# Performance work log

Hardware: AMD Instinct MI355X
Metric: run time of the kernel (lower is better)

Reference implementation:

```python
import jax, jax.numpy as jnp
import numpy as np

T, B, OBS, H, A = 512, 256, 128, 256, 32

def setup_inputs() -> dict:
    key = jax.random.key(0)
    ks = jax.random.split(key, 16)
    s = 0.05
    return {
        'hidden': jnp.zeros((B, H), jnp.float32),
        'obs': jax.random.normal(ks[0], (T, B, OBS), jnp.float32),
        'dones': jax.random.bernoulli(ks[1], 0.1, (T, B)),
        'avail_actions': (jax.random.uniform(ks[2], (T, B, A)) > 0.1).astype(jnp.float32),
        'W_emb': jax.random.normal(ks[3], (OBS, H), jnp.float32) * s,
        'b_emb': jnp.zeros((H,), jnp.float32),
        'Wi': jax.random.normal(ks[4], (H, 3 * H), jnp.float32) * s,
        'bi': jnp.zeros((3 * H,), jnp.float32),
        'Whr': jax.random.normal(ks[5], (H, H), jnp.float32) * s,
        'Whz': jax.random.normal(ks[6], (H, H), jnp.float32) * s,
        'Whn': jax.random.normal(ks[7], (H, H), jnp.float32) * s,
        'bhn': jnp.zeros((H,), jnp.float32),
        'W_a1': jax.random.normal(ks[8], (H, H), jnp.float32) * s,
        'b_a1': jnp.zeros((H,), jnp.float32),
        'W_a2': jax.random.normal(ks[9], (H, A), jnp.float32) * s,
        'b_a2': jnp.zeros((A,), jnp.float32),
        'W_c1': jax.random.normal(ks[10], (H, H), jnp.float32) * s,
        'b_c1': jnp.zeros((H,), jnp.float32),
        'W_c2': jax.random.normal(ks[11], (H, 1), jnp.float32) * s,
        'b_c2': jnp.zeros((1,), jnp.float32),
    }

def reference(hidden, obs, dones, avail_actions, W_emb, b_emb, Wi, bi,
              Whr, Whz, Whn, bhn, W_a1, b_a1, W_a2, b_a2, W_c1, b_c1, W_c2, b_c2):
    # obs embedding + relu: [T,B,OBS] -> [T,B,H]
    emb = jax.nn.relu(obs @ W_emb + b_emb)
    # precompute input gate projections for all timesteps (same math as per-step Dense)
    gi = emb @ Wi + bi  # [T,B,3H]

    def step(h, xs):
        gi_t, done_t = xs
        h = jnp.where(done_t[:, None], 0.0, h)  # reset-select to zero init carry
        ir, iz, inn = jnp.split(gi_t, 3, axis=-1)
        r = jax.nn.sigmoid(ir + h @ Whr)
        z = jax.nn.sigmoid(iz + h @ Whz)
        n = jnp.tanh(inn + r * (h @ Whn + bhn))
        h_new = (1.0 - z) * n + z * h
        return h_new, h_new

    hidden_out, y = jax.lax.scan(step, hidden, (gi, dones))  # y: [T,B,H]

    actor_h = jax.nn.relu(y @ W_a1 + b_a1)
    actor_mean = actor_h @ W_a2 + b_a2  # [T,B,A]
    logits = actor_mean - (1.0 - avail_actions) * 1e10

    critic_h = jax.nn.relu(y @ W_c1 + b_c1)
    value = jnp.squeeze(critic_h @ W_c2 + b_c2, axis=-1)  # [T,B]
    return hidden_out, logits, value
```

## Files before the change

### kernel.cpp

```cpp
#include <hip/hip_runtime.h>
#include <stdint.h>

#define T_DIM 512
#define B_DIM 256
#define OBS_DIM 128
#define H_DIM 256
#define A_DIM 32
#define TB (T_DIM*B_DIM)

typedef unsigned short u16;
typedef unsigned int   u32;
typedef _Float16 half2v __attribute__((ext_vector_type(2)));
typedef __attribute__((ext_vector_type(8))) short short8;
typedef __attribute__((ext_vector_type(4))) float f32x4;
typedef __attribute__((ext_vector_type(4))) u32   u32x4;

__device__ __forceinline__ float bf2f(u16 v){ return __uint_as_float(((u32)v)<<16); }
__device__ __forceinline__ u16 f2bf(float f){
    u32 x = __float_as_uint(f);
    u32 r = x + 0x7fffu + ((x>>16)&1u);
    return (u16)(r>>16);
}
__device__ __forceinline__ float2 bfpair(u32 u){
    return make_float2(__uint_as_float(u<<16), __uint_as_float(u & 0xffff0000u));
}

__device__ __forceinline__ float dot2(u32 a, u32 b, float c){
#if __has_builtin(__builtin_amdgcn_fdot2)
    return __builtin_amdgcn_fdot2(__builtin_bit_cast(half2v,a),
                                  __builtin_bit_cast(half2v,b), c, false);
#else
    half2v ha = __builtin_bit_cast(half2v,a), hb = __builtin_bit_cast(half2v,b);
    return fmaf((float)ha[0],(float)hb[0], fmaf((float)ha[1],(float)hb[1], c));
#endif
}

__global__ void zero_flags_kernel(int* p){ if(threadIdx.x<4) p[threadIdx.x]=0; }

__global__ void detect_kernel(const unsigned char* __restrict__ d, int n, int* __restrict__ flags){
    int f=0;
    for(int p = blockIdx.x*blockDim.x+threadIdx.x; p<n; p += gridDim.x*blockDim.x){
        if(d[p]){ int m=p&3; if(m==1) f|=1; else if(m>=2) f|=2; }
    }
    if(f) atomicOr(flags, f);
}

__global__ void concat_bias_kernel(const float* __restrict__ a, const float* __restrict__ b,
                                   float* __restrict__ dst){
    int i = threadIdx.x;
    dst[i] = a[i];
    dst[256 + i] = b[i];
}

__global__ void cvt_wt_kernel(const float* __restrict__ Whr, const float* __restrict__ Whz,
                              const float* __restrict__ Whn, u32* __restrict__ dst){
    int i = blockIdx.x*blockDim.x + threadIdx.x;
    if(i >= 3*32*256*4) return;
    int e = i & 3;
    int j = (i >> 2) & 255;
    int q = (i >> 10) & 31;
    int m = i >> 15;
    const float* W = (m==0) ? Whr : (m==1) ? Whz : Whn;
    int kp = q*4 + e, k = 2*kp;
    _Float16 lo = (_Float16)W[(size_t)k    *H_DIM + j];
    _Float16 hi = (_Float16)W[(size_t)(k+1)*H_DIM + j];
    dst[i] = (u32)__builtin_bit_cast(u16,lo) | ((u32)__builtin_bit_cast(u16,hi) << 16);
}

__global__ void cvt_wT_kernel(const float* __restrict__ W, u16* __restrict__ dst,
                              int K, int N){
    int i = blockIdx.x*blockDim.x + threadIdx.x;
    if(i >= K*N) return;
    int n = i / K;
    int k = i - n*K;
    dst[i] = f2bf(W[(size_t)k*N + n]);
}

template<int RELU, int AF32>
__global__ __launch_bounds__(256, 2)
void gemm_mfma_kernel(const void* __restrict__ A_, const u16* __restrict__ Bt,
                      const float* __restrict__ bias, u16* __restrict__ C,
                      int M, int N, int K)
{
    __shared__ u16 As[128*32];
    __shared__ u16 Bs[128*32];
    const int tid  = threadIdx.x;
    const int wave = tid >> 6;
    const int lane = tid & 63;
    const int ln15 = lane & 15;
    const int quad = lane >> 4;
    const int wm = wave & 1, wn = wave >> 1;
    const int rowBase = blockIdx.y*128;
    const int colBase = blockIdx.x*128;

    f32x4 acc[4][4] = {};

    const int sr = tid >> 1;
    const int sc = (tid & 1) * 16;

    for(int kb = 0; kb < K; kb += 32){
        if(AF32){
            const float* af = (const float*)A_;
            const float* ag = af + (size_t)(rowBase+sr)*K + kb + sc;
            float4 f0 = *(const float4*)ag;
            float4 f1 = *(const float4*)(ag+4);
            float4 f2 = *(const float4*)(ag+8);
            float4 f3 = *(const float4*)(ag+12);
            u16 tmp[16] = { f2bf(f0.x),f2bf(f0.y),f2bf(f0.z),f2bf(f0.w),
                            f2bf(f1.x),f2bf(f1.y),f2bf(f1.z),f2bf(f1.w),
                            f2bf(f2.x),f2bf(f2.y),f2bf(f2.z),f2bf(f2.w),
                            f2bf(f3.x),f2bf(f3.y),f2bf(f3.z),f2bf(f3.w) };
            *(uint4*)&As[sr*32 + sc]     = *(const uint4*)&tmp[0];
            *(uint4*)&As[sr*32 + sc + 8] = *(const uint4*)&tmp[8];
        } else {
            const u16* ab = (const u16*)A_;
            const u16* ag = ab + (size_t)(rowBase+sr)*K + kb + sc;
            uint4 av0 = *(const uint4*)ag;
            uint4 av1 = *(const uint4*)(ag+8);
            *(uint4*)&As[sr*32 + sc]     = av0;
            *(uint4*)&As[sr*32 + sc + 8] = av1;
        }
        {
            const u16* bg = Bt + (size_t)(colBase+sr)*K + kb + sc;
            uint4 bv0 = *(const uint4*)bg;
            uint4 bv1 = *(const uint4*)(bg+8);
            *(uint4*)&Bs[sr*32 + sc]     = bv0;
            *(uint4*)&Bs[sr*32 + sc + 8] = bv1;
        }
        __syncthreads();

        short8 af[4], bf[4];
        #pragma unroll
        for(int mt=0;mt<4;mt++)
            af[mt] = *(const short8*)&As[(wm*64+mt*16+ln15)*32 + quad*8];
        #pragma unroll
        for(int nt=0;nt<4;nt++)
            bf[nt] = *(const short8*)&Bs[(wn*64+nt*16+ln15)*32 + quad*8];
        #pragma unroll
        for(int mt=0;mt<4;mt++){
            #pragma unroll
            for(int nt=0;nt<4;nt++){
                acc[mt][nt] = __builtin_amdgcn_mfma_f32_16x16x32_bf16(
                                  af[mt], bf[nt], acc[mt][nt], 0, 0, 0);
            }
        }
        __syncthreads();
    }

    #pragma unroll
    for(int nt=0;nt<4;nt++){
        int n = colBase + wn*64 + nt*16 + ln15;
        float bv = bias[n];
        #pragma unroll
        for(int mt=0;mt<4;mt++){
            #pragma unroll
            for(int r=0;r<4;r++){
                int m = rowBase + wm*64 + mt*16 + quad*4 + r;
                float v = acc[mt][nt][r] + bv;
                if(RELU) v = fmaxf(v, 0.f);
                C[(size_t)m*N + n] = f2bf(v);
            }
        }
    }
}

__global__ __attribute__((amdgpu_flat_work_group_size(1024,1024), amdgpu_waves_per_eu(4,4)))
void scan_kernel(const u16* __restrict__ gi, const void* __restrict__ dones,
                 const int* __restrict__ flags, const u32x4* __restrict__ Wt4,
                 const float* __restrict__ bhn, float* __restrict__ h_carry,
                 u16* __restrict__ y, int t0, int Tc)
{
    __shared__ __align__(16) u32 nw_lds[32*256*4/4*4];
    __shared__ __align__(16) u32 hbuf[2][128];
    __shared__ float rex[3][4][256];
    const int tid = threadIdx.x;
    const int j   = tid & 255;
    const int g   = tid >> 8;
    const int row = blockIdx.x;
    const int fl  = flags[0];
    const int mode = (fl&1) ? 0 : ((fl&2) ? 2 : 1);

    auto getdone = [&](int t)->bool{
        int idx = t*B_DIM + row;
        if(mode==0) return ((const unsigned char*)dones)[idx] != 0;
        if(mode==1) return ((const int*)dones)[idx] != 0;
        return ((const float*)dones)[idx] != 0.f;
    };

    const u32x4* baseR = Wt4 + (size_t)( 0 + g*8)*256 + j;
    const u32x4* baseZ = Wt4 + (size_t)(32 + g*8)*256 + j;
    const u32x4* baseN = Wt4 + (size_t)(64 + g*8)*256 + j;
    u32 wr[32], wz[32];
    #pragma unroll
    for(int q=0;q<8;q++){
        u32x4 tr = baseR[(size_t)q*256]; wr[4*q]=tr[0]; wr[4*q+1]=tr[1]; wr[4*q+2]=tr[2]; wr[4*q+3]=tr[3];
        u32x4 tz = baseZ[(size_t)q*256]; wz[4*q]=tz[0]; wz[4*q+1]=tz[1]; wz[4*q+2]=tz[2]; wz[4*q+3]=tz[3];
    }
    {
        u32x4* nl = (u32x4*)nw_lds;
        #pragma unroll
        for(int q=0;q<8;q++)
            nl[(size_t)(g*8+q)*256 + j] = baseN[(size_t)q*256];
    }
    #pragma unroll
    for(int q=0;q<32;q+=4){
        asm volatile("" : "+v"(wr[q  ]),"+v"(wr[q+1]),"+v"(wr[q+2]),"+v"(wr[q+3]),
                          "+v"(wz[q  ]),"+v"(wz[q+1]),"+v"(wz[q+2]),"+v"(wz[q+3]));
    }

    float bh = 0.f;
    float hoj = 0.f;
    if(g == 0){
        bh = bhn[j];
        bool d0 = getdone(t0);
        hoj = d0 ? 0.f : h_carry[(size_t)row*H_DIM + j];
        ((_Float16*)hbuf[0])[j] = (_Float16)hoj;
    }
    __syncthreads();

    int cur = 0;
    for(int t=0; t<Tc; ++t){
        size_t gbase = ((size_t)t*B_DIM + row)*768;
        float ir=0.f, izv=0.f, inn=0.f; bool dn=false;
        if(g == 0){
            ir  = bf2f(gi[gbase + j]);
            izv = bf2f(gi[gbase + 256 + j]);
            inn = bf2f(gi[gbase + 512 + j]);
            dn  = (t < Tc-1) ? getdone(t0+t+1) : false;
        }

        float r0=0.f,r1=0.f,z0=0.f,z1=0.f,n0=0.f,n1=0.f;
        const u32x4* hb = (const u32x4*)hbuf[cur] + g*8;
        const u32x4* nb = (const u32x4*)nw_lds + (size_t)(g*8)*256 + j;
        #pragma unroll
        for(int q=0;q<8;q++){
            u32x4 hv = hb[q];
            u32x4 nv = nb[(size_t)q*256];
            r0 = dot2(wr[4*q  ], hv[0], r0); r1 = dot2(wr[4*q+1], hv[1], r1);
            r0 = dot2(wr[4*q+2], hv[2], r0); r1 = dot2(wr[4*q+3], hv[3], r1);
            z0 = dot2(wz[4*q  ], hv[0], z0); z1 = dot2(wz[4*q+1], hv[1], z1);
            z0 = dot2(wz[4*q+2], hv[2], z0); z1 = dot2(wz[4*q+3], hv[3], z1);
            n0 = dot2(nv[0], hv[0], n0); n1 = dot2(nv[1], hv[1], n1);
            n0 = dot2(nv[2], hv[2], n0); n1 = dot2(nv[3], hv[3], n1);
        }
        rex[0][g][j] = r0 + r1;
        rex[1][g][j] = z0 + z1;
        rex[2][g][j] = n0 + n1;
        __syncthreads();

        if(g == 0){
            float rt = (rex[0][0][j] + rex[0][1][j]) + (rex[0][2][j] + rex[0][3][j]);
            float zt = (rex[1][0][j] + rex[1][1][j]) + (rex[1][2][j] + rex[1][3][j]);
            float nt = (rex[2][0][j] + rex[2][1][j]) + (rex[2][2][j] + rex[2][3][j]);
            float r = 1.f/(1.f + __expf(-(ir + rt)));
            float z = 1.f/(1.f + __expf(-(izv + zt)));
            float x = inn + r*(nt + bh);
            float e2 = __expf(2.f*x);
            float n = 1.f - 2.f/(e2 + 1.f);
            float hn = (1.f - z)*n + z*hoj;
            y[((size_t)t*B_DIM + row)*H_DIM + j] = f2bf(hn);
            hoj = dn ? 0.f : hn;
            ((_Float16*)hbuf[cur^1])[j] = (_Float16)hoj;
        }
        __syncthreads();
        cur ^= 1;
    }

    if(g == 0) h_carry[(size_t)row*H_DIM + j] = hoj;
}

__global__ __launch_bounds__(256)
void actor2_kernel(const u16* __restrict__ ah, int ld, const float* __restrict__ W_a2,
                   const float* __restrict__ b_a2, const float* __restrict__ avail,
                   float* __restrict__ logits)
{
    __shared__ u16 ahs[64][264];
    const int tid = threadIdx.x;
    const int r0 = blockIdx.x*64;
    {
        int row = tid & 63;
        int c0 = (tid >> 6) * 64;
        const uint4* gp = (const uint4*)(ah + (size_t)(r0+row)*ld + c0);
        #pragma unroll
        for(int q=0;q<8;q++){
            uint4 u = gp[q];
            u32* dst = (u32*)&ahs[row][c0 + q*8];
            dst[0]=u.x; dst[1]=u.y; dst[2]=u.z; dst[3]=u.w;
        }
    }
    __syncthreads();
    const int c  = tid & 31;
    const int rg = tid >> 5;
    float acc[8]={0.f,0.f,0.f,0.f,0.f,0.f,0.f,0.f};
    float bc = b_a2[c];
    for(int k=0;k<H_DIM;k+=4){
        float w0 = W_a2[(k+0)*A_DIM + c];
        float w1 = W_a2[(k+1)*A_DIM + c];
        float w2 = W_a2[(k+2)*A_DIM + c];
        float w3 = W_a2[(k+3)*A_DIM + c];
        #pragma unroll
        for(int rr=0;rr<8;rr++){
            uint2 av = *(const uint2*)&ahs[rg*8+rr][k];
            float2 p0 = bfpair(av.x), p1 = bfpair(av.y);
            acc[rr] = fmaf(p0.x,w0,fmaf(p0.y,w1,fmaf(p1.x,w2,fmaf(p1.y,w3,acc[rr]))));
        }
    }
    #pragma unroll
    for(int rr=0;rr<8;rr++){
        int grow = r0 + rg*8 + rr;
        float av = avail[(size_t)grow*A_DIM + c];
        logits[(size_t)grow*A_DIM + c] = acc[rr] + bc - (1.f-av)*1e10f;
    }
}

__global__ __launch_bounds__(256)
void critic2_kernel(const u16* __restrict__ ch, int ld, const float* __restrict__ W_c2,
                    const float* __restrict__ b_c2, float* __restrict__ value)
{
    const int lane = threadIdx.x & 63;
    const int wid  = threadIdx.x >> 6;
    const int row  = blockIdx.x*4 + wid;
    uint2 av = *(const uint2*)(ch + (size_t)row*ld + lane*4);
    float2 p0 = bfpair(av.x), p1 = bfpair(av.y);
    float4 wv = *(const float4*)(W_c2 + lane*4);
    float acc = p0.x*wv.x + p0.y*wv.y + p1.x*wv.z + p1.y*wv.w;
    #pragma unroll
    for(int off=32; off>0; off>>=1) acc += __shfl_down(acc, off, 64);
    if(lane==0) value[row] = acc + b_c2[0];
}

extern "C" void kernel_launch(void* const* d_in, const int* in_sizes, int n_in,
                              void* d_out, int out_size, void* d_ws, size_t ws_size,
                              hipStream_t stream)
{
    const float* hidden = (const float*)d_in[0];
    const float* obs    = (const float*)d_in[1];
    const void*  dones  = d_in[2];
    const float* avail  = (const float*)d_in[3];
    const float* W_emb  = (const float*)d_in[4];
    const float* b_emb  = (const float*)d_in[5];
    const float* Wi     = (const float*)d_in[6];
    const float* bi     = (const float*)d_in[7];
    const float* Whr    = (const float*)d_in[8];
    const float* Whz    = (const float*)d_in[9];
    const float* Whn    = (const float*)d_in[10];
    const float* bhn    = (const float*)d_in[11];
    const float* W_a1   = (const float*)d_in[12];
    const float* b_a1   = (const float*)d_in[13];
    const float* W_a2   = (const float*)d_in[14];
    const float* b_a2   = (const float*)d_in[15];
    const float* W_c1   = (const float*)d_in[16];
    const float* b_c1   = (const float*)d_in[17];
    const float* W_c2   = (const float*)d_in[18];
    const float* b_c2   = (const float*)d_in[19];

    float* out_hidden = (float*)d_out;
    float* out_logits = out_hidden + (size_t)B_DIM*H_DIM;
    float* out_value  = out_logits + (size_t)TB*A_DIM;

    const size_t fixed = 393216 + 393216 + 262144 + 65536 + 262144 + 256 + 2048;
    int Tc = 4;
    for(int cand = 64; cand >= 4; cand >>= 1){
        size_t need = fixed + (size_t)cand*(393216  + 262144  + 131072 );
        if(need <= ws_size){ Tc = cand; break; }
    }
    const int NC = T_DIM / Tc;

    uint8_t* ws = (uint8_t*)d_ws;
    size_t off = 0;
    u32*  wt_b    = (u32*)(ws + off); off += 393216;
    u16*  wiT     = (u16*)(ws + off); off += 393216;
    u16*  wacT    = (u16*)(ws + off); off += 262144;
    u16*  wembT   = (u16*)(ws + off); off += 65536;
    float* h_carry= (float*)(ws + off); off += 262144;
    int*  flags   = (int*)(ws + off); off += 256;
    float* b_ac   = (float*)(ws + off); off += 2048;
    u16*  gi_c    = (u16*)(ws + off); off += (size_t)Tc*393216;
    u16*  embac_c = (u16*)(ws + off); off += (size_t)Tc*262144;
    u16*  y_c     = (u16*)(ws + off); off += (size_t)Tc*131072;
    u16*  emb_c   = embac_c;
    u16*  ac_c    = embac_c;

    zero_flags_kernel<<<1, 64, 0, stream>>>(flags);
    detect_kernel<<<64, 256, 0, stream>>>((const unsigned char*)dones, TB, flags);
    cvt_wt_kernel<<<384, 256, 0, stream>>>(Whr, Whz, Whn, wt_b);
    cvt_wT_kernel<<<768, 256, 0, stream>>>(Wi,   wiT,  256, 768);
    cvt_wT_kernel<<<256, 256, 0, stream>>>(W_a1, wacT,          256, 256);
    cvt_wT_kernel<<<256, 256, 0, stream>>>(W_c1, wacT + 65536,  256, 256);
    cvt_wT_kernel<<<128, 256, 0, stream>>>(W_emb, wembT, 128, 256);
    concat_bias_kernel<<<1, 256, 0, stream>>>(b_a1, b_c1, b_ac);
    hipMemcpyAsync(h_carry, hidden, (size_t)B_DIM*H_DIM*sizeof(float),
                   hipMemcpyDeviceToDevice, stream);

    const int Mc = Tc*B_DIM;
    const int gy = Mc/128;

    for(int c = 0; c < NC; ++c){
        const int t0 = c*Tc;
        const float* obs_c = obs + (size_t)t0*B_DIM*OBS_DIM;
        gemm_mfma_kernel<1,1><<<dim3(2,gy), 256, 0, stream>>>(obs_c, wembT, b_emb, emb_c, Mc, 256, 128);
        gemm_mfma_kernel<0,0><<<dim3(6,gy), 256, 0, stream>>>(emb_c, wiT, bi, gi_c, Mc, 768, 256);
        scan_kernel<<<256, 1024, 0, stream>>>(gi_c, dones, flags, (const u32x4*)wt_b,
                                              bhn, h_carry, y_c, t0, Tc);
        gemm_mfma_kernel<1,0><<<dim3(4,gy), 256, 0, stream>>>(y_c, wacT, b_ac, ac_c, Mc, 512, 256);
        actor2_kernel<<<Mc/64, 256, 0, stream>>>(ac_c, 512, W_a2, b_a2,
                                                 avail + (size_t)t0*B_DIM*A_DIM,
                                                 out_logits + (size_t)t0*B_DIM*A_DIM);
        critic2_kernel<<<Mc/4, 256, 0, stream>>>(ac_c + 256, 512, W_c2, b_c2,
                                                 out_value + (size_t)t0*B_DIM);
    }

    hipMemcpyAsync(out_hidden, h_carry, (size_t)B_DIM*H_DIM*sizeof(float),
                   hipMemcpyDeviceToDevice, stream);
}
```

Baseline: 1.360 ms.

## Use MFMA for GRU recurrent matmul with four batch rows per block

Replaces the per-row scan kernel's fdot2 matvec, which holds weights in registers and LDS, with MFMA 16x16x32 f16 instructions. Each block now processes four batch rows, padded to a 16-row tile in LDS with an XOR swizzle, and all recurrent weights stay in registers. The aim is to cut per-step latency and the number of blocks by amortising weight use across rows on the matrix cores. In exchange, 12 of the 16 MFMA rows are wasted, only 64 blocks run, and a new transposed f16 weight conversion is needed.

Result: slower. 1.936 ms (+42.4%).

```diff
diff --git a/kernel.cpp b/kernel.cpp
--- a/kernel.cpp
+++ b/kernel.cpp
@@ -7,10 +7,12 @@
 #define H_DIM 256
 #define A_DIM 32
 #define TB (T_DIM*B_DIM)
+#define SR 4
 
 typedef unsigned short u16;
 typedef unsigned int   u32;
 typedef _Float16 half2v __attribute__((ext_vector_type(2)));
+typedef _Float16 f16x8 __attribute__((ext_vector_type(8)));
 typedef __attribute__((ext_vector_type(8))) short short8;
 typedef __attribute__((ext_vector_type(4))) float f32x4;
 typedef __attribute__((ext_vector_type(4))) u32   u32x4;
@@ -25,16 +27,6 @@
     return make_float2(__uint_as_float(u<<16), __uint_as_float(u & 0xffff0000u));
 }
 
-__device__ __forceinline__ float dot2(u32 a, u32 b, float c){
-#if __has_builtin(__builtin_amdgcn_fdot2)
-    return __builtin_amdgcn_fdot2(__builtin_bit_cast(half2v,a),
-                                  __builtin_bit_cast(half2v,b), c, false);
-#else
-    half2v ha = __builtin_bit_cast(half2v,a), hb = __builtin_bit_cast(half2v,b);
-    return fmaf((float)ha[0],(float)hb[0], fmaf((float)ha[1],(float)hb[1], c));
-#endif
-}
-
 __global__ void zero_flags_kernel(int* p){ if(threadIdx.x<4) p[threadIdx.x]=0; }
 
 __global__ void detect_kernel(const unsigned char* __restrict__ d, int n, int* __restrict__ flags){
@@ -52,19 +44,15 @@
     dst[256 + i] = b[i];
 }
 
-__global__ void cvt_wt_kernel(const float* __restrict__ Whr, const float* __restrict__ Whz,
-                              const float* __restrict__ Whn, u32* __restrict__ dst){
+__global__ void cvt_wT3_f16_kernel(const float* __restrict__ Whr, const float* __restrict__ Whz,
+                                   const float* __restrict__ Whn, _Float16* __restrict__ dst){
     int i = blockIdx.x*blockDim.x + threadIdx.x;
-    if(i >= 3*32*256*4) return;
-    int e = i & 3;
-    int j = (i >> 2) & 255;
-    int q = (i >> 10) & 31;
-    int m = i >> 15;
+    if(i >= 3*H_DIM*H_DIM) return;
+    int k = i & 255;
+    int j = (i >> 8) & 255;
+    int m = i >> 16;
     const float* W = (m==0) ? Whr : (m==1) ? Whz : Whn;
-    int kp = q*4 + e, k = 2*kp;
-    _Float16 lo = (_Float16)W[(size_t)k    *H_DIM + j];
-    _Float16 hi = (_Float16)W[(size_t)(k+1)*H_DIM + j];
-    dst[i] = (u32)__builtin_bit_cast(u16,lo) | ((u32)__builtin_bit_cast(u16,hi) << 16);
+    dst[i] = (_Float16)W[(size_t)k*H_DIM + j];
 }
 
 __global__ void cvt_wT_kernel(const float* __restrict__ W, u16* __restrict__ dst,
@@ -164,109 +152,124 @@
     }
 }
 
-__global__ __attribute__((amdgpu_flat_work_group_size(1024,1024), amdgpu_waves_per_eu(4,4)))
+__global__ __attribute__((amdgpu_flat_work_group_size(512,512), amdgpu_waves_per_eu(2,2)))
 void scan_kernel(const u16* __restrict__ gi, const void* __restrict__ dones,
-                 const int* __restrict__ flags, const u32x4* __restrict__ Wt4,
+                 const int* __restrict__ flags, const _Float16* __restrict__ WT,
                  const float* __restrict__ bhn, float* __restrict__ h_carry,
                  u16* __restrict__ y, int t0, int Tc)
 {
-    __shared__ __align__(16) u32 nw_lds[32*256*4/4*4];
-    __shared__ __align__(16) u32 hbuf[2][128];
-    __shared__ float rex[3][4][256];
-    const int tid = threadIdx.x;
-    const int j   = tid & 255;
-    const int g   = tid >> 8;
-    const int row = blockIdx.x;
-    const int fl  = flags[0];
+    __shared__ _Float16 h_lds[16*256];
+    __shared__ float accb[3][256][6];
+    __shared__ unsigned char dn_lds[64][SR];
+
+    const int tid  = threadIdx.x;
+    const int wave = tid >> 6;
+    const int lane = tid & 63;
+    const int ln15 = lane & 15;
+    const int quad = lane >> 4;
+    const int rb   = blockIdx.x * SR;
+    const int fl   = flags[0];
     const int mode = (fl&1) ? 0 : ((fl&2) ? 2 : 1);
 
-    auto getdone = [&](int t)->bool{
-        int idx = t*B_DIM + row;
-        if(mode==0) return ((const unsigned char*)dones)[idx] != 0;
-        if(mode==1) return ((const int*)dones)[idx] != 0;
-        return ((const float*)dones)[idx] != 0.f;
-    };
-
-    const u32x4* baseR = Wt4 + (size_t)( 0 + g*8)*256 + j;
-    const u32x4* baseZ = Wt4 + (size_t)(32 + g*8)*256 + j;
-    const u32x4* baseN = Wt4 + (size_t)(64 + g*8)*256 + j;
-    u32 wr[32], wz[32];
+    f16x8 wf[2][3][8];
+    {
+        const f16x8* Wv = (const f16x8*)WT;
+        #pragma unroll
+        for(int s=0;s<2;s++){
+            int col = (wave*2+s)*16 + ln15;
+            #pragma unroll
+            for(int m=0;m<3;m++){
+                #pragma unroll
+                for(int kk=0;kk<8;kk++)
+                    wf[s][m][kk] = Wv[(size_t)(m*256 + col)*32 + kk*4 + quad];
+            }
+        }
+    }
+
+    if(tid < Tc*SR){
+        int tt = tid >> 2, r = tid & 3;
+        int idx = (t0+tt)*B_DIM + rb + r;
+        bool d;
+        if(mode==0)      d = ((const unsigned char*)dones)[idx] != 0;
+        else if(mode==1) d = ((const int*)dones)[idx] != 0;
+        else             d = ((const float*)dones)[idx] != 0.f;
+        dn_lds[tt][r] = d ? 1 : 0;
+    }
+    for(int i = 1024 + tid; i < 4096; i += 512) h_lds[i] = (_Float16)0.f;
+    __syncthreads();
+
+    const int col = tid & 255;
+    const int rp  = tid >> 8;
+    const float bh = bhn[col];
+    float hreg[2];
     #pragma unroll
-    for(int q=0;q<8;q++){
-        u32x4 tr = baseR[(size_t)q*256]; wr[4*q]=tr[0]; wr[4*q+1]=tr[1]; wr[4*q+2]=tr[2]; wr[4*q+3]=tr[3];
-        u32x4 tz = baseZ[(size_t)q*256]; wz[4*q]=tz[0]; wz[4*q+1]=tz[1]; wz[4*q+2]=tz[2]; wz[4*q+3]=tz[3];
-    }
-    {
-        u32x4* nl = (u32x4*)nw_lds;
-        #pragma unroll
-        for(int q=0;q<8;q++)
-            nl[(size_t)(g*8+q)*256 + j] = baseN[(size_t)q*256];
-    }
-    #pragma unroll
-    for(int q=0;q<32;q+=4){
-        asm volatile("" : "+v"(wr[q  ]),"+v"(wr[q+1]),"+v"(wr[q+2]),"+v"(wr[q+3]),
-                          "+v"(wz[q  ]),"+v"(wz[q+1]),"+v"(wz[q+2]),"+v"(wz[q+3]));
-    }
-
-    float bh = 0.f;
-    float hoj = 0.f;
-    if(g == 0){
-        bh = bhn[j];
-        bool d0 = getdone(t0);
-        hoj = d0 ? 0.f : h_carry[(size_t)row*H_DIM + j];
-        ((_Float16*)hbuf[0])[j] = (_Float16)hoj;
+    for(int e=0;e<2;e++){
+        int row = rp*2 + e;
+        bool d0 = dn_lds[0][row] != 0;
+        hreg[e] = d0 ? 0.f : h_carry[(size_t)(rb+row)*H_DIM + col];
+        h_lds[row*256 + (((col>>3) ^ row)<<3) + (col&7)] = (_Float16)hreg[e];
     }
     __syncthreads();
 
-    int cur = 0;
     for(int t=0; t<Tc; ++t){
-        size_t gbase = ((size_t)t*B_DIM + row)*768;
-        float ir=0.f, izv=0.f, inn=0.f; bool dn=false;
-        if(g == 0){
-            ir  = bf2f(gi[gbase + j]);
-            izv = bf2f(gi[gbase + 256 + j]);
-            inn = bf2f(gi[gbase + 512 + j]);
-            dn  = (t < Tc-1) ? getdone(t0+t+1) : false;
-        }
-
-        float r0=0.f,r1=0.f,z0=0.f,z1=0.f,n0=0.f,n1=0.f;
-        const u32x4* hb = (const u32x4*)hbuf[cur] + g*8;
-        const u32x4* nb = (const u32x4*)nw_lds + (size_t)(g*8)*256 + j;
-        #pragma unroll
-        for(int q=0;q<8;q++){
-            u32x4 hv = hb[q];
-            u32x4 nv = nb[(size_t)q*256];
-            r0 = dot2(wr[4*q  ], hv[0], r0); r1 = dot2(wr[4*q+1], hv[1], r1);
-            r0 = dot2(wr[4*q+2], hv[2], r0); r1 = dot2(wr[4*q+3], hv[3], r1);
-            z0 = dot2(wz[4*q  ], hv[0], z0); z1 = dot2(wz[4*q+1], hv[1], z1);
-            z0 = dot2(wz[4*q+2], hv[2], z0); z1 = dot2(wz[4*q+3], hv[3], z1);
-            n0 = dot2(nv[0], hv[0], n0); n1 = dot2(nv[1], hv[1], n1);
-            n0 = dot2(nv[2], hv[2], n0); n1 = dot2(nv[3], hv[3], n1);
-        }
-        rex[0][g][j] = r0 + r1;
-        rex[1][g][j] = z0 + z1;
-        rex[2][g][j] = n0 + n1;
+        size_t gb = ((size_t)t*B_DIM + rb)*768;
+        float giv[2][3];
+        #pragma unroll
+        for(int e=0;e<2;e++){
+            size_t ro = gb + (size_t)(rp*2+e)*768;
+            giv[e][0] = bf2f(gi[ro + col]);
+            giv[e][1] = bf2f(gi[ro + 256 + col]);
+            giv[e][2] = bf2f(gi[ro + 512 + col]);
+        }
+
+        f32x4 acc[2][3] = {};
+        #pragma unroll
+        for(int kk=0;kk<8;kk++){
+            f16x8 hv = *(const f16x8*)&h_lds[ln15*256 + (((kk*4+quad) ^ (ln15&7))<<3)];
+            #pragma unroll
+            for(int s=0;s<2;s++){
+                acc[s][0] = __builtin_amdgcn_mfma_f32_16x16x32_f16(hv, wf[s][0][kk], acc[s][0], 0,0,0);
+                acc[s][1] = __builtin_amdgcn_mfma_f32_16x16x32_f16(hv, wf[s][1][kk], acc[s][1], 0,0,0);
+                acc[s][2] = __builtin_amdgcn_mfma_f32_16x16x32_f16(hv, wf[s][2][kk], acc[s][2], 0,0,0);
+            }
+        }
+
+        if(quad == 0){
+            #pragma unroll
+            for(int s=0;s<2;s++){
+                int c = (wave*2+s)*16 + ln15;
+                #pragma unroll
+                for(int m=0;m<3;m++){
+                    *(float2*)&accb[m][c][0] = make_float2(acc[s][m][0], acc[s][m][1]);
+                    *(float2*)&accb[m][c][2] = make_float2(acc[s][m][2], acc[s][m][3]);
+                }
+            }
+        }
         __syncthreads();
 
-        if(g == 0){
-            float rt = (rex[0][0][j] + rex[0][1][j]) + (rex[0][2][j] + rex[0][3][j]);
-            float zt = (rex[1][0][j] + rex[1][1][j]) + (rex[1][2][j] + rex[1][3][j]);
-            float nt = (rex[2][0][j] + rex[2][1][j]) + (rex[2][2][j] + rex[2][3][j]);
-            float r = 1.f/(1.f + __expf(-(ir + rt)));
-            float z = 1.f/(1.f + __expf(-(izv + zt)));
-            float x = inn + r*(nt + bh);
+        #pragma unroll
+        for(int e=0;e<2;e++){
+            int row = rp*2 + e;
+            float rt  = accb[0][col][row];
+            float zt  = accb[1][col][row];
+            float ntv = accb[2][col][row];
+            float r = 1.f/(1.f + __expf(-(giv[e][0] + rt)));
+            float z = 1.f/(1.f + __expf(-(giv[e][1] + zt)));
+            float x = giv[e][2] + r*(ntv + bh);
             float e2 = __expf(2.f*x);
             float n = 1.f - 2.f/(e2 + 1.f);
-            float hn = (1.f - z)*n + z*hoj;
-            y[((size_t)t*B_DIM + row)*H_DIM + j] = f2bf(hn);
-            hoj = dn ? 0.f : hn;
-            ((_Float16*)hbuf[cur^1])[j] = (_Float16)hoj;
+            float hn = (1.f - z)*n + z*hreg[e];
+            y[((size_t)t*B_DIM + rb + row)*H_DIM + col] = f2bf(hn);
+            bool dn = (t < Tc-1) ? (dn_lds[t+1][row] != 0) : false;
+            hreg[e] = dn ? 0.f : hn;
+            h_lds[row*256 + (((col>>3) ^ row)<<3) + (col&7)] = (_Float16)hreg[e];
         }
         __syncthreads();
-        cur ^= 1;
-    }
-
-    if(g == 0) h_carry[(size_t)row*H_DIM + j] = hoj;
+    }
+
+    #pragma unroll
+    for(int e=0;e<2;e++)
+        h_carry[(size_t)(rb + rp*2 + e)*H_DIM + col] = hreg[e];
 }
 
 __global__ __launch_bounds__(256)
@@ -368,7 +371,7 @@
 
     uint8_t* ws = (uint8_t*)d_ws;
     size_t off = 0;
-    u32*  wt_b    = (u32*)(ws + off); off += 393216;
+    _Float16* wT  = (_Float16*)(ws + off); off += 393216;
     u16*  wiT     = (u16*)(ws + off); off += 393216;
     u16*  wacT    = (u16*)(ws + off); off += 262144;
     u16*  wembT   = (u16*)(ws + off); off += 65536;
@@ -383,7 +386,7 @@
 
     zero_flags_kernel<<<1, 64, 0, stream>>>(flags);
     detect_kernel<<<64, 256, 0, stream>>>((const unsigned char*)dones, TB, flags);
-    cvt_wt_kernel<<<384, 256, 0, stream>>>(Whr, Whz, Whn, wt_b);
+    cvt_wT3_f16_kernel<<<768, 256, 0, stream>>>(Whr, Whz, Whn, wT);
     cvt_wT_kernel<<<768, 256, 0, stream>>>(Wi,   wiT,  256, 768);
     cvt_wT_kernel<<<256, 256, 0, stream>>>(W_a1, wacT,          256, 256);
     cvt_wT_kernel<<<256, 256, 0, stream>>>(W_c1, wacT + 65536,  256, 256);
@@ -400,8 +403,8 @@
         const float* obs_c = obs + (size_t)t0*B_DIM*OBS_DIM;
         gemm_mfma_kernel<1,1><<<dim3(2,gy), 256, 0, stream>>>(obs_c, wembT, b_emb, emb_c, Mc, 256, 128);
         gemm_mfma_kernel<0,0><<<dim3(6,gy), 256, 0, stream>>>(emb_c, wiT, bi, gi_c, Mc, 768, 256);
-        scan_kernel<<<256, 1024, 0, stream>>>(gi_c, dones, flags, (const u32x4*)wt_b,
-                                              bhn, h_carry, y_c, t0, Tc);
+        scan_kernel<<<B_DIM/SR, 512, 0, stream>>>(gi_c, dones, flags, wT,
+                                                  bhn, h_carry, y_c, t0, Tc);
         gemm_mfma_kernel<1,0><<<dim3(4,gy), 256, 0, stream>>>(y_c, wacT, b_ac, ac_c, Mc, 512, 256);
         actor2_kernel<<<Mc/64, 256, 0, stream>>>(ac_c, 512, W_a2, b_a2,
                                                  avail + (size_t)t0*B_DIM*A_DIM,
```

## Hold all GRU recurrent weights in registers with one thread per hidden unit

Applied to the files above, without the earlier changes.

The scan kernel drops from 1024 threads per block, which split the K dimension across four groups and combined partials through shared memory, to 256 threads that each keep all 384 packed weight words for their column in VGPRs. This removes the LDS partial-sum reduction, the per-step LDS reads of the n-gate weights and one of the two barriers per timestep. In exchange each thread does four times the dot-product work serially, and the 384-plus live weight registers may spill or force a single wave per SIMD with little latency hiding.

Measured after the change: 1.955 ms. 43.8% more time.

```diff
diff --git a/kernel.cpp b/kernel.cpp
--- a/kernel.cpp
+++ b/kernel.cpp
@@ -164,18 +164,14 @@
     }
 }
 
-__global__ __attribute__((amdgpu_flat_work_group_size(1024,1024), amdgpu_waves_per_eu(4,4)))
+__global__ __attribute__((amdgpu_flat_work_group_size(256,256), amdgpu_waves_per_eu(1,1)))
 void scan_kernel(const u16* __restrict__ gi, const void* __restrict__ dones,
                  const int* __restrict__ flags, const u32x4* __restrict__ Wt4,
                  const float* __restrict__ bhn, float* __restrict__ h_carry,
                  u16* __restrict__ y, int t0, int Tc)
 {
-    __shared__ __align__(16) u32 nw_lds[32*256*4/4*4];
     __shared__ __align__(16) u32 hbuf[2][128];
-    __shared__ float rex[3][4][256];
-    const int tid = threadIdx.x;
-    const int j   = tid & 255;
-    const int g   = tid >> 8;
+    const int j   = threadIdx.x;
     const int row = blockIdx.x;
     const int fl  = flags[0];
     const int mode = (fl&1) ? 0 : ((fl&2) ? 2 : 1);
@@ -187,31 +183,26 @@
         return ((const float*)dones)[idx] != 0.f;
     };
 
-    const u32x4* baseR = Wt4 + (size_t)( 0 + g*8)*256 + j;
-    const u32x4* baseZ = Wt4 + (size_t)(32 + g*8)*256 + j;
-    const u32x4* baseN = Wt4 + (size_t)(64 + g*8)*256 + j;
-    u32 wr[32], wz[32];
-    #pragma unroll
-    for(int q=0;q<8;q++){
+    const u32x4* baseR = Wt4 + (size_t)( 0)*256 + j;
+    const u32x4* baseZ = Wt4 + (size_t)(32)*256 + j;
+    const u32x4* baseN = Wt4 + (size_t)(64)*256 + j;
+    u32 wr[128], wz[128], wn[128];
+    #pragma unroll
+    for(int q=0;q<32;q++){
         u32x4 tr = baseR[(size_t)q*256]; wr[4*q]=tr[0]; wr[4*q+1]=tr[1]; wr[4*q+2]=tr[2]; wr[4*q+3]=tr[3];
         u32x4 tz = baseZ[(size_t)q*256]; wz[4*q]=tz[0]; wz[4*q+1]=tz[1]; wz[4*q+2]=tz[2]; wz[4*q+3]=tz[3];
-    }
+        u32x4 tn = baseN[(size_t)q*256]; wn[4*q]=tn[0]; wn[4*q+1]=tn[1]; wn[4*q+2]=tn[2]; wn[4*q+3]=tn[3];
+    }
+    #pragma unroll
+    for(int q=0;q<128;q+=4){
+        asm volatile("" : "+v"(wr[q  ]),"+v"(wr[q+1]),"+v"(wr[q+2]),"+v"(wr[q+3]),
+                          "+v"(wz[q  ]),"+v"(wz[q+1]),"+v"(wz[q+2]),"+v"(wz[q+3]),
+                          "+v"(wn[q  ]),"+v"(wn[q+1]),"+v"(wn[q+2]),"+v"(wn[q+3]));
+    }
+
+    const float bh = bhn[j];
+    float hoj;
     {
-        u32x4* nl = (u32x4*)nw_lds;
-        #pragma unroll
-        for(int q=0;q<8;q++)
-            nl[(size_t)(g*8+q)*256 + j] = baseN[(size_t)q*256];
-    }
-    #pragma unroll
-    for(int q=0;q<32;q+=4){
-        asm volatile("" : "+v"(wr[q  ]),"+v"(wr[q+1]),"+v"(wr[q+2]),"+v"(wr[q+3]),
-                          "+v"(wz[q  ]),"+v"(wz[q+1]),"+v"(wz[q+2]),"+v"(wz[q+3]));
-    }
-
-    float bh = 0.f;
-    float hoj = 0.f;
-    if(g == 0){
-        bh = bhn[j];
         bool d0 = getdone(t0);
         hoj = d0 ? 0.f : h_carry[(size_t)row*H_DIM + j];
         ((_Float16*)hbuf[0])[j] = (_Float16)hoj;
@@ -221,52 +212,38 @@
     int cur = 0;
     for(int t=0; t<Tc; ++t){
         size_t gbase = ((size_t)t*B_DIM + row)*768;
-        float ir=0.f, izv=0.f, inn=0.f; bool dn=false;
-        if(g == 0){
-            ir  = bf2f(gi[gbase + j]);
-            izv = bf2f(gi[gbase + 256 + j]);
-            inn = bf2f(gi[gbase + 512 + j]);
-            dn  = (t < Tc-1) ? getdone(t0+t+1) : false;
-        }
+        float ir  = bf2f(gi[gbase + j]);
+        float izv = bf2f(gi[gbase + 256 + j]);
+        float inn = bf2f(gi[gbase + 512 + j]);
+        bool  dn  = (t < Tc-1) ? getdone(t0+t+1) : false;
 
         float r0=0.f,r1=0.f,z0=0.f,z1=0.f,n0=0.f,n1=0.f;
-        const u32x4* hb = (const u32x4*)hbuf[cur] + g*8;
-        const u32x4* nb = (const u32x4*)nw_lds + (size_t)(g*8)*256 + j;
-        #pragma unroll
-        for(int q=0;q<8;q++){
+        const u32x4* hb = (const u32x4*)hbuf[cur];
+        #pragma unroll
+        for(int q=0;q<32;q++){
             u32x4 hv = hb[q];
-            u32x4 nv = nb[(size_t)q*256];
             r0 = dot2(wr[4*q  ], hv[0], r0); r1 = dot2(wr[4*q+1], hv[1], r1);
             r0 = dot2(wr[4*q+2], hv[2], r0); r1 = dot2(wr[4*q+3], hv[3], r1);
             z0 = dot2(wz[4*q  ], hv[0], z0); z1 = dot2(wz[4*q+1], hv[1], z1);
             z0 = dot2(wz[4*q+2], hv[2], z0); z1 = dot2(wz[4*q+3], hv[3], z1);
-            n0 = dot2(nv[0], hv[0], n0); n1 = dot2(nv[1], hv[1], n1);
-            n0 = dot2(nv[2], hv[2], n0); n1 = dot2(nv[3], hv[3], n1);
-        }
-        rex[0][g][j] = r0 + r1;
-        rex[1][g][j] = z0 + z1;
-        rex[2][g][j] = n0 + n1;
-        __syncthreads();
-
-        if(g == 0){
-            float rt = (rex[0][0][j] + rex[0][1][j]) + (rex[0][2][j] + rex[0][3][j]);
-            float zt = (rex[1][0][j] + rex[1][1][j]) + (rex[1][2][j] + rex[1][3][j]);
-            float nt = (rex[2][0][j] + rex[2][1][j]) + (rex[2][2][j] + rex[2][3][j]);
-            float r = 1.f/(1.f + __expf(-(ir + rt)));
-            float z = 1.f/(1.f + __expf(-(izv + zt)));
-            float x = inn + r*(nt + bh);
-            float e2 = __expf(2.f*x);
-            float n = 1.f - 2.f/(e2 + 1.f);
-            float hn = (1.f - z)*n + z*hoj;
-            y[((size_t)t*B_DIM + row)*H_DIM + j] = f2bf(hn);
-            hoj = dn ? 0.f : hn;
-            ((_Float16*)hbuf[cur^1])[j] = (_Float16)hoj;
-        }
+            n0 = dot2(wn[4*q  ], hv[0], n0); n1 = dot2(wn[4*q+1], hv[1], n1);
+            n0 = dot2(wn[4*q+2], hv[2], n0); n1 = dot2(wn[4*q+3], hv[3], n1);
+        }
+
+        float r = 1.f/(1.f + __expf(-(ir  + r0 + r1)));
+        float z = 1.f/(1.f + __expf(-(izv + z0 + z1)));
+        float x = inn + r*(n0 + n1 + bh);
+        float e2 = __expf(2.f*x);
+        float n = 1.f - 2.f/(e2 + 1.f);
+        float hn = (1.f - z)*n + z*hoj;
+        y[((size_t)t*B_DIM + row)*H_DIM + j] = f2bf(hn);
+        hoj = dn ? 0.f : hn;
+        ((_Float16*)hbuf[cur^1])[j] = (_Float16)hoj;
         __syncthreads();
         cur ^= 1;
     }
 
-    if(g == 0) h_carry[(size_t)row*H_DIM + j] = hoj;
+    h_carry[(size_t)row*H_DIM + j] = hoj;
 }
 
 __global__ __launch_bounds__(256)
@@ -400,8 +377,8 @@
         const float* obs_c = obs + (size_t)t0*B_DIM*OBS_DIM;
         gemm_mfma_kernel<1,1><<<dim3(2,gy), 256, 0, stream>>>(obs_c, wembT, b_emb, emb_c, Mc, 256, 128);
         gemm_mfma_kernel<0,0><<<dim3(6,gy), 256, 0, stream>>>(emb_c, wiT, bi, gi_c, Mc, 768, 256);
-        scan_kernel<<<256, 1024, 0, stream>>>(gi_c, dones, flags, (const u32x4*)wt_b,
-                                              bhn, h_carry, y_c, t0, Tc);
+        scan_kernel<<<256, 256, 0, stream>>>(gi_c, dones, flags, (const u32x4*)wt_b,
+                                             bhn, h_carry, y_c, t0, Tc);
         gemm_mfma_kernel<1,0><<<dim3(4,gy), 256, 0, stream>>>(y_c, wacT, b_ac, ac_c, Mc, 512, 256);
         actor2_kernel<<<Mc/64, 256, 0, stream>>>(ac_c, 512, W_a2, b_a2,
                                                  avail + (size_t)t0*B_DIM*A_DIM,
```
